# Kernel optimization log

Measured on AMD Instinct MI355X. Metric: run time of the kernel, lower is better.

Reference implementation:

```python
import jax, jax.numpy as jnp
import numpy as np

B, H, W = 16, 16, 16
L = 32          # in_capsules
O = 32          # out_capsules
P = 16          # p_size
PD = 4          # p_dim = sqrt(p_size)
ETA = 1.0


def setup_inputs() -> dict:
    key = jax.random.key(0)
    k1, k2, k3 = jax.random.split(key, 3)
    # [B, H, W, L*(P+1)]: first L*P channels are poses, last L are activations in [0,1]
    input_tensor = jax.random.uniform(k1, (B, H, W, L * (P + 1)), dtype=jnp.float32)
    # transform weights: [L, O, 4, 4] (kernel_size=1, shared over spatial positions)
    weights = jax.random.normal(k2, (L, O, PD, PD), dtype=jnp.float32) / np.sqrt(PD)
    activation_bias = jax.random.uniform(k3, (O,), dtype=jnp.float32)
    return {"input_tensor": input_tensor, "weights": weights,
            "activation_bias": activation_bias}


def reference(input_tensor, weights, activation_bias):
    Bs, Hh, Ww, _ = input_tensor.shape
    M = Hh * Ww
    # split poses / activations
    poses = input_tensor[..., : L * P].reshape(Bs, M, L, PD, PD)   # [B, M, L, 4, 4]
    acts = input_tensor[..., L * P:].reshape(Bs, M * L)            # [B, N]
    # votes[b, (m,l), o] = pose[b,m,l] @ W[l,o]  (shared transform, repeated over M)
    votes = jnp.einsum('bmlij,lojk->bmloik', poses, weights)
    votes = votes.reshape(Bs, M * L, O, P)                         # [B, N, O, 16]
    # weight votes by input activations and group per output capsule
    Y = (acts[:, :, None, None] * votes).transpose(0, 2, 1, 3)     # [B, O, N, 16]
    # top-1 right singular vector via gram matrix eigendecomposition (detached)
    gram = jnp.einsum('bonp,bonq->bopq', Y, Y)                     # [B, O, 16, 16]
    _, V = jnp.linalg.eigh(jax.lax.stop_gradient(gram))            # ascending eigvals
    pose_out = V[..., -1]                                          # [B, O, 16]
    # agreement: ||Y u||^2 / ||Y||_F^2
    yu = jnp.einsum('bonp,bop->bon', Y, pose_out)                  # [B, O, N]
    ratio = (yu ** 2).sum(-1) / (Y ** 2).sum((-1, -2))             # [B, O]
    act_out = jax.nn.sigmoid(ETA * (ratio - activation_bias))      # [B, O]
    return act_out, pose_out
```

## Files before the change

### kernel.cpp

```cpp
#include <hip/hip_runtime.h>

#define B_ 16
#define L_ 32
#define O_ 32
#define M_ 256
#define CH_ 544


__device__ __forceinline__ float rl(float v, int lane) {
  return __int_as_float(__builtin_amdgcn_readlane(__float_as_int(v), lane));
}

__device__ __forceinline__ float sum16_rl(float v) {
  float s = rl(v, 0);
#pragma unroll
  for (int j = 1; j < 16; j++) s += rl(v, j);
  return s;
}

__device__ __forceinline__ float frcp(float x) { return __builtin_amdgcn_rcpf(x); }
__device__ __forceinline__ float frsq(float x) { return __builtin_amdgcn_rsqf(x); }


__device__ __forceinline__ float slapy2f(float x, float y) {
  float xa = fabsf(x), ya = fabsf(y);
  float w = fmaxf(xa, ya), z = fminf(xa, ya);
  if (z == 0.f) return w;
  float q = z * frcp(w);
  return w * sqrtf(1.f + q * q);
}

__device__ __forceinline__ void slartgf(float f, float g, float* c, float* s, float* r) {
  if (g == 0.f) { *c = 1.f; *s = 0.f; *r = f; }
  else if (f == 0.f) { *c = 0.f; *s = copysignf(1.f, g); *r = fabsf(g); }
  else {
    float t = f * f + g * g;
    float inv = frsq(t);
    float d = t * inv;
    *c = fabsf(f) * inv;
    *r = copysignf(d, f);
    *s = g * copysignf(inv, f);
  }
}

__device__ __forceinline__ void slaev2f(float a, float b, float c,
                                        float* rt1, float* rt2, float* cs1, float* sn1) {
  float sm = a + c, df = a - c;
  float adf = fabsf(df);
  float tb = b + b;
  float ab = fabsf(tb);
  float acmx, acmn;
  if (fabsf(a) > fabsf(c)) { acmx = a; acmn = c; } else { acmx = c; acmn = a; }
  float rt;
  if (adf > ab) { float q = ab / adf; rt = adf * sqrtf(1.f + q * q); }
  else if (adf < ab) { float q = adf / ab; rt = ab * sqrtf(1.f + q * q); }
  else rt = ab * sqrtf(2.f);
  int sgn1;
  if (sm < 0.f) { *rt1 = 0.5f * (sm - rt); sgn1 = -1; *rt2 = (acmx / *rt1) * acmn - (b / *rt1) * b; }
  else if (sm > 0.f) { *rt1 = 0.5f * (sm + rt); sgn1 = 1; *rt2 = (acmx / *rt1) * acmn - (b / *rt1) * b; }
  else { *rt1 = 0.5f * rt; *rt2 = -0.5f * rt; sgn1 = 1; }
  float cs; int sgn2;
  if (df >= 0.f) { cs = df + rt; sgn2 = 1; } else { cs = df - rt; sgn2 = -1; }
  float acs = fabsf(cs), c1, s1;
  if (acs > ab) { float ct = -tb / cs; s1 = 1.f / sqrtf(1.f + ct * ct); c1 = ct * s1; }
  else if (ab == 0.f) { c1 = 1.f; s1 = 0.f; }
  else { float tn = -cs / tb; c1 = 1.f / sqrtf(1.f + tn * tn); s1 = tn * c1; }
  if (sgn1 == sgn2) { float tn = c1; c1 = -s1; s1 = tn; }
  *cs1 = c1; *sn1 = s1;
}

__global__ __launch_bounds__(256) void moments_kernel(const float* __restrict__ in,
                                                      float* __restrict__ Tmom) {
  int bl = blockIdx.x;
  int b = bl >> 5, l = bl & 31;
  int t = threadIdx.x;
  int w = t >> 6, lane = t & 63;
  __shared__ __align__(16) float ut[4][16][68];
  const float* base = in + (size_t)b * (M_ * CH_);
  const float* row = base + (size_t)(w * 64 + lane) * CH_ + l * 16;
  float4 p0 = *(const float4*)(row + 0);
  float4 p1 = *(const float4*)(row + 4);
  float4 p2 = *(const float4*)(row + 8);
  float4 p3 = *(const float4*)(row + 12);
  float a = row[512 - l * 16 + l];
  float (*u)[68] = ut[w];
  u[0][lane] = a * p0.x;  u[1][lane] = a * p0.y;  u[2][lane] = a * p0.z;  u[3][lane] = a * p0.w;
  u[4][lane] = a * p1.x;  u[5][lane] = a * p1.y;  u[6][lane] = a * p1.z;  u[7][lane] = a * p1.w;
  u[8][lane] = a * p2.x;  u[9][lane] = a * p2.y;  u[10][lane] = a * p2.z; u[11][lane] = a * p2.w;
  u[12][lane] = a * p3.x; u[13][lane] = a * p3.y; u[14][lane] = a * p3.z; u[15][lane] = a * p3.w;
  asm volatile("" ::: "memory");
  int c = lane & 15, r0 = lane >> 4;
  float acc0 = 0.f, acc1 = 0.f, acc2 = 0.f, acc3 = 0.f;
#pragma unroll
  for (int m4 = 0; m4 < 64; m4 += 4) {
    float4 cv = *(const float4*)&u[c][m4];
    float4 a0 = *(const float4*)&u[r0][m4];
    float4 a1 = *(const float4*)&u[r0 + 4][m4];
    float4 a2 = *(const float4*)&u[r0 + 8][m4];
    float4 a3 = *(const float4*)&u[r0 + 12][m4];
    acc0 += a0.x * cv.x + a0.y * cv.y + a0.z * cv.z + a0.w * cv.w;
    acc1 += a1.x * cv.x + a1.y * cv.y + a1.z * cv.z + a1.w * cv.w;
    acc2 += a2.x * cv.x + a2.y * cv.y + a2.z * cv.z + a2.w * cv.w;
    acc3 += a3.x * cv.x + a3.y * cv.y + a3.z * cv.z + a3.w * cv.w;
  }
  float* dst = Tmom + ((size_t)bl * 4 + w) * 256;
  dst[r0 * 16 + c] = acc0;
  dst[(r0 + 4) * 16 + c] = acc1;
  dst[(r0 + 8) * 16 + c] = acc2;
  dst[(r0 + 12) * 16 + c] = acc3;
}

__global__ __launch_bounds__(64) void gram_eig_kernel(const float* __restrict__ Tmom,
                                                      const float* __restrict__ Wt,
                                                      const float* __restrict__ bias,
                                                      float* __restrict__ out) {
  int bo = blockIdx.x;
  int b = bo >> 5, o = bo & 31;
  int lane = threadIdx.x;

  __shared__ __align__(16) float4 Wall4[128];
  __shared__ __align__(16) float4 Tsh4[4 * 18];
  __shared__ float A[16][17];
  __shared__ __align__(16) float Zt[16][16];

  const float4* Wt4 = (const float4*)Wt;
#pragma unroll
  for (int k = 0; k < 2; k++) {
    int idx = lane + 64 * k;
    int l = idx >> 2, part = idx & 3;
    Wall4[idx] = Wt4[(l * 32 + o) * 4 + part];
  }
  asm volatile("" ::: "memory");

  int p = lane >> 2;
  int i_ = p >> 2, k_ = p & 3;
  int i2 = lane & 3;
  float gx = 0.f, gy = 0.f, gz = 0.f, gw = 0.f;
  const float4* T4b = (const float4*)Tmom + (size_t)(b * 32) * 4 * 64;
  const float* WallF = (const float*)Wall4;
  float4 tc0 = T4b[0 * 64 + lane], tc1 = T4b[1 * 64 + lane];
  float4 tc2 = T4b[2 * 64 + lane], tc3 = T4b[3 * 64 + lane];
  float4 tn0 = T4b[4 * 64 + lane], tn1 = T4b[5 * 64 + lane];
  float4 tn2 = T4b[6 * 64 + lane], tn3 = T4b[7 * 64 + lane];
  for (int l = 0; l < 32; l++) {
    float4 tsum;
    tsum.x = (tc0.x + tc1.x) + (tc2.x + tc3.x);
    tsum.y = (tc0.y + tc1.y) + (tc2.y + tc3.y);
    tsum.z = (tc0.z + tc1.z) + (tc2.z + tc3.z);
    tsum.w = (tc0.w + tc1.w) + (tc2.w + tc3.w);
    Tsh4[(lane >> 4) * 18 + (lane & 15)] = tsum;
    asm volatile("" ::: "memory");
    tc0 = tn0; tc1 = tn1; tc2 = tn2; tc3 = tn3;
    if (l + 2 < 32) {
      const float4* nb = T4b + (size_t)(l + 2) * 4 * 64;
      tn0 = nb[0 * 64 + lane]; tn1 = nb[1 * 64 + lane];
      tn2 = nb[2 * 64 + lane]; tn3 = nb[3 * 64 + lane];
    }
    float4 wq0 = Wall4[l * 4 + 0], wq1 = Wall4[l * 4 + 1];
    float4 wq2 = Wall4[l * 4 + 2], wq3 = Wall4[l * 4 + 3];
#pragma unroll
    for (int jj = 0; jj < 4; jj++) {
      float4 trow = Tsh4[i_ * 18 + jj * 4 + i2];
      float ux = trow.x * wq0.x + trow.y * wq1.x + trow.z * wq2.x + trow.w * wq3.x;
      float uy = trow.x * wq0.y + trow.y * wq1.y + trow.z * wq2.y + trow.w * wq3.y;
      float uz = trow.x * wq0.z + trow.y * wq1.z + trow.z * wq2.z + trow.w * wq3.z;
      float uw = trow.x * wq0.w + trow.y * wq1.w + trow.z * wq2.w + trow.w * wq3.w;
      float wk = WallF[l * 16 + jj * 4 + k_];
      gx += wk * ux; gy += wk * uy; gz += wk * uz; gw += wk * uw;
    }
    asm volatile("" ::: "memory");
  }
  {
    int q0 = i2 * 4;
    A[p][q0 + 0] = gx; A[p][q0 + 1] = gy; A[p][q0 + 2] = gz; A[p][q0 + 3] = gw;
  }
  asm volatile("" ::: "memory");

  int c16 = lane & 15;
  float a[16];
#pragma unroll
  for (int r = 0; r < 16; r++) a[r] = A[r][c16];

  float trace;
  {
    float diag = 0.f;
#pragma unroll
    for (int r = 0; r < 16; r++) if (c16 == r) diag = a[r];
    trace = sum16_rl((lane < 16) ? diag : 0.f);
  }

  float dreg = 0.f, ereg = 0.f, taureg = 0.f;
  float hv[14];
#pragma unroll
  for (int i = 0; i < 15; i++) {
    float cn = 0.f;
#pragma unroll
    for (int r = i + 2; r < 16; r++) cn += a[r] * a[r];
    float xn2 = rl(cn, i);
    float alpha = rl(a[i + 1], i);
    float taui = 0.f;
    float vc = 0.f;
    if (xn2 == 0.f) {
      if (lane == i) ereg = alpha;
    } else {
      float xnorm = sqrtf(xn2);
      float beta = -copysignf(slapy2f(alpha, xnorm), alpha);
      taui = (beta - alpha) / beta;
      float rs = 1.f / (alpha - beta);
      if (lane == i) ereg = beta;
      vc = (lane == i + 1) ? 1.f : ((lane >= i + 2 && lane < 16) ? a[i] * rs : 0.f);
      float vb[16];
#pragma unroll
      for (int r = i + 1; r < 16; r++) vb[r] = rl(vc, r);
      float acc = 0.f;
#pragma unroll
      for (int r = i + 1; r < 16; r++) acc += a[r] * vb[r];
      float wc = (lane >= i + 1 && lane < 16) ? taui * acc : 0.f;
      float wb[16];
#pragma unroll
      for (int r = i + 1; r < 16; r++) wb[r] = rl(wc, r);
      float dot = 0.f;
#pragma unroll
      for (int r = i + 1; r < 16; r++) dot += vb[r] * wb[r];
      float alph2 = -0.5f * taui * dot;
      wc += alph2 * vc;
#pragma unroll
      for (int r = i + 1; r < 16; r++) wb[r] += alph2 * vb[r];
#pragma unroll
      for (int r = i + 1; r < 16; r++) a[r] -= vb[r] * wc + wb[r] * vc;
    }
    if (i < 14) hv[i] = vc;
    if (lane == i) taureg = taui;
  }
#pragma unroll
  for (int r = 0; r < 16; r++) if (c16 == r) dreg = a[r];
  if (lane >= 16) dreg = 0.f;

  float z[16];
#pragma unroll
  for (int r = 0; r < 16; r++) z[r] = (lane == r) ? 1.f : 0.f;
#pragma unroll
  for (int i = 13; i >= 0; i--) {
    float taui = rl(taureg, i);
    if (taui != 0.f) {
      float vbq[16];
      float s = 0.f;
#pragma unroll
      for (int r = i + 1; r < 16; r++) { vbq[r] = rl(hv[i], r); s += vbq[r] * z[r]; }
      s *= taui;
#pragma unroll
      for (int r = i + 1; r < 16; r++) z[r] -= vbq[r] * s;
    }
  }
  if (lane < 16) {
    float4* zt4 = (float4*)&Zt[lane][0];
    zt4[0] = make_float4(z[0], z[1], z[2], z[3]);
    zt4[1] = make_float4(z[4], z[5], z[6], z[7]);
    zt4[2] = make_float4(z[8], z[9], z[10], z[11]);
    zt4[3] = make_float4(z[12], z[13], z[14], z[15]);
  }
  asm volatile("" ::: "memory");

  const float eps = 5.9604645e-08f;
  const float eps2 = eps * eps;
  const float safmin = 1.17549435e-38f;
  int l1 = 0, jtot = 0;
  const int nmaxit = 480;
  float dsh = __shfl(dreg, (lane + 1) & 63, 64);

  while (l1 < 16) {
    if (l1 > 0) { if (lane == l1 - 1) ereg = 0.f; }
    bool co = (lane < 15) &&
              ((ereg == 0.f) ||
               (fabsf(ereg) <= __builtin_amdgcn_sqrtf(fabsf(dreg)) *
                                   __builtin_amdgcn_sqrtf(fabsf(dsh)) * eps));
    unsigned long long bm = __ballot(co) & ~((1ull << l1) - 1ull);
    int m = bm ? (__ffsll(bm) - 1) : 15;
    if (m < 15) { if (lane == m) ereg = 0.f; }
    int l = l1, lend = m;
    l1 = m + 1;
    if (lend == l) continue;
    {
      float dl = rl(dreg, l), dle = rl(dreg, lend);
      if (fabsf(dle) < fabsf(dl)) { int tq = l; l = lend; lend = tq; }
    }

    if (lend > l) {
      for (;;) {
        bool cj = (lane < 15) && ((ereg * ereg) <= eps2 * fabsf(dreg) * fabsf(dsh) + safmin);
        int mq;
        if (l != lend) {
          unsigned long long bb2 = __ballot(cj) & ((1ull << lend) - 1ull) & ~((1ull << l) - 1ull);
          mq = bb2 ? (__ffsll(bb2) - 1) : lend;
        } else mq = lend;
        if (mq < lend) { if (lane == mq) ereg = 0.f; }
        if (mq == l) { l++; if (l <= lend) continue; break; }
        if (mq == l + 1) {
          float d_l = rl(dreg, l), e_l = rl(ereg, l), d_l1 = rl(dreg, l + 1);
          float rt1, rt2, cc, ss;
          slaev2f(d_l, e_l, d_l1, &rt1, &rt2, &cc, &ss);
          if (lane < 16) {
            float z1 = Zt[l + 1][lane], z0 = Zt[l][lane];
            Zt[l + 1][lane] = cc * z1 - ss * z0;
            Zt[l][lane] = ss * z1 + cc * z0;
          }
          if (lane == l) { dreg = rt1; ereg = 0.f; dsh = rt2; }
          if (lane == l + 1) dreg = rt2;
          if (lane == l - 1) dsh = rt1;
          l += 2; if (l <= lend) continue; break;
        }
        if (jtot == nmaxit) break;
        jtot++;
        float d0 = dreg, e0 = ereg;
        float pp = rl(d0, l);
        float e_lv = rl(e0, l);
        float gg = (rl(d0, l + 1) - pp) * 0.5f * frcp(e_lv);
        float rr = slapy2f(gg, 1.f);
        gg = rl(d0, mq) - pp + e_lv * frcp(gg + copysignf(rr, gg));
        float ss_ = 1.f, cc_ = 1.f;
        pp = 0.f;
        float zc = (lane < 16) ? Zt[mq][lane] : 0.f;
        float znxt = (lane < 16) ? Zt[mq - 1][lane] : 0.f;
        for (int i = mq - 1; i >= l; i--) {
          float z0 = znxt;
          if (i > l) znxt = (lane < 16) ? Zt[i - 1][lane] : 0.f;
          float e_i = rl(e0, i), d_i = rl(d0, i), d_i1 = rl(d0, i + 1);
          float ff = ss_ * e_i, bb = cc_ * e_i;
          slartgf(gg, ff, &cc_, &ss_, &rr);
          if (i != mq - 1) { if (lane == i + 1) ereg = rr; }
          gg = d_i1 - pp;
          rr = (d_i - gg) * ss_ + 2.f * cc_ * bb;
          pp = ss_ * rr;
          float dnew = gg + pp;
          if (lane == i + 1) dreg = dnew;
          if (lane == i) dsh = dnew;
          gg = cc_ * rr - bb;
          if (lane < 16) Zt[i + 1][lane] = cc_ * zc + ss_ * z0;
          zc = -ss_ * zc + cc_ * z0;
        }
        if (lane < 16) Zt[l][lane] = zc;
        float dlv = rl(d0, l) - pp;
        if (lane == l) { dreg = dlv; ereg = gg; }
        if (lane == l - 1) dsh = dlv;
      }
    } else {
      for (;;) {
        bool cj = (lane < 15) && ((ereg * ereg) <= eps2 * fabsf(dreg) * fabsf(dsh) + safmin);
        int mq;
        if (l != lend) {
          unsigned long long bb2 = __ballot(cj) & ((1ull << l) - 1ull) & ~((1ull << lend) - 1ull);
          mq = bb2 ? (63 - __clzll(bb2) + 1) : lend;
        } else mq = lend;
        if (mq > lend) { if (lane == mq - 1) ereg = 0.f; }
        if (mq == l) { l--; if (l >= lend) continue; break; }
        if (mq == l - 1) {
          float d_lm1 = rl(dreg, l - 1), e_lm1 = rl(ereg, l - 1), d_l = rl(dreg, l);
          float rt1, rt2, cc, ss;
          slaev2f(d_lm1, e_lm1, d_l, &rt1, &rt2, &cc, &ss);
          if (lane < 16) {
            float z1 = Zt[l][lane], z0 = Zt[l - 1][lane];
            Zt[l][lane] = cc * z1 - ss * z0;
            Zt[l - 1][lane] = ss * z1 + cc * z0;
          }
          if (lane == l - 1) { dreg = rt1; ereg = 0.f; dsh = rt2; }
          if (lane == l) dreg = rt2;
          if (lane == l - 2) dsh = rt1;
          l -= 2; if (l >= lend) continue; break;
        }
        if (jtot == nmaxit) break;
        jtot++;
        float d0 = dreg, e0 = ereg;
        float pp = rl(d0, l);
        float e_lm1 = rl(e0, l - 1);
        float gg = (rl(d0, l - 1) - pp) * 0.5f * frcp(e_lm1);
        float rr = slapy2f(gg, 1.f);
        gg = rl(d0, mq) - pp + e_lm1 * frcp(gg + copysignf(rr, gg));
        float ss_ = 1.f, cc_ = 1.f;
        pp = 0.f;
        float zc = (lane < 16) ? Zt[mq][lane] : 0.f;
        float znxt = (lane < 16) ? Zt[mq + 1][lane] : 0.f;
        for (int i = mq; i <= l - 1; i++) {
          float z1 = znxt;
          if (i < l - 1) znxt = (lane < 16) ? Zt[i + 2][lane] : 0.f;
          float e_i = rl(e0, i), d_i = rl(d0, i), d_i1 = rl(d0, i + 1);
          float ff = ss_ * e_i, bb = cc_ * e_i;
          slartgf(gg, ff, &cc_, &ss_, &rr);
          if (i != mq) { if (lane == i - 1) ereg = rr; }
          gg = d_i - pp;
          rr = (d_i1 - gg) * ss_ + 2.f * cc_ * bb;
          pp = ss_ * rr;
          float dnew = gg + pp;
          if (lane == i) dreg = dnew;
          if (lane == i - 1) dsh = dnew;
          gg = cc_ * rr - bb;
          if (lane < 16) Zt[i][lane] = ss_ * z1 + cc_ * zc;
          zc = cc_ * z1 - ss_ * zc;
        }
        if (lane < 16) Zt[l][lane] = zc;
        float dlv = rl(d0, l) - pp;
        if (lane == l) dreg = dlv;
        if (lane == l - 1) { ereg = gg; dsh = dlv; }
      }
    }
  }
  asm volatile("" ::: "memory");

  float mx = rl(dreg, 0);
  int k = 0;
#pragma unroll
  for (int j = 1; j < 16; j++) {
    float dj = rl(dreg, j);
    if (dj > mx) { mx = dj; k = j; }
  }
  float ratio = mx / trace;
  float act = 1.f / (1.f + expf(-(ratio - bias[o])));
  if (lane < 16) out[512 + bo * 16 + lane] = Zt[k][lane];
  if (lane == 0) out[bo] = act;
}

extern "C" void kernel_launch(void* const* d_in, const int* in_sizes, int n_in,
                              void* d_out, int out_size, void* d_ws, size_t ws_size,
                              hipStream_t stream) {
  const float* in = (const float*)d_in[0];
  const float* w = (const float*)d_in[1];
  const float* bias = (const float*)d_in[2];
  float* out = (float*)d_out;
  float* Tmom = (float*)d_ws;

  moments_kernel<<<B_ * L_, 256, 0, stream>>>(in, Tmom);
  gram_eig_kernel<<<B_ * O_, 64, 0, stream>>>(Tmom, w, bias, out);
}
```

Baseline: 132.6 us.

## Keep eigenvector matrix in registers, reduce moment partials in-block, branchless Givens

```diff
diff --git a/kernel.cpp b/kernel.cpp
--- a/kernel.cpp
+++ b/kernel.cpp
@@ -25,22 +25,22 @@
 __device__ __forceinline__ float slapy2f(float x, float y) {
   float xa = fabsf(x), ya = fabsf(y);
   float w = fmaxf(xa, ya), z = fminf(xa, ya);
-  if (z == 0.f) return w;
   float q = z * frcp(w);
-  return w * sqrtf(1.f + q * q);
+  float res = w * sqrtf(1.f + q * q);
+  return (z == 0.f) ? w : res;
 }
 
 __device__ __forceinline__ void slartgf(float f, float g, float* c, float* s, float* r) {
-  if (g == 0.f) { *c = 1.f; *s = 0.f; *r = f; }
-  else if (f == 0.f) { *c = 0.f; *s = copysignf(1.f, g); *r = fabsf(g); }
-  else {
-    float t = f * f + g * g;
-    float inv = frsq(t);
-    float d = t * inv;
-    *c = fabsf(f) * inv;
-    *r = copysignf(d, f);
-    *s = g * copysignf(inv, f);
-  }
+  float t = f * f + g * g;
+  float inv = frsq(t);
+  float d = t * inv;
+  float cg = fabsf(f) * inv;
+  float rg = copysignf(d, f);
+  float sg = g * copysignf(inv, f);
+  bool g0 = (g == 0.f), f0 = (f == 0.f);
+  *c = g0 ? 1.f : (f0 ? 0.f : cg);
+  *s = g0 ? 0.f : (f0 ? copysignf(1.f, g) : sg);
+  *r = g0 ? f : (f0 ? fabsf(g) : rg);
 }
 
 __device__ __forceinline__ void slaev2f(float a, float b, float c,
@@ -76,6 +76,7 @@
   int t = threadIdx.x;
   int w = t >> 6, lane = t & 63;
   __shared__ __align__(16) float ut[4][16][68];
+  __shared__ float red[4][16][16];
   const float* base = in + (size_t)b * (M_ * CH_);
   const float* row = base + (size_t)(w * 64 + lane) * CH_ + l * 16;
   float4 p0 = *(const float4*)(row + 0);
@@ -103,11 +104,14 @@
     acc2 += a2.x * cv.x + a2.y * cv.y + a2.z * cv.z + a2.w * cv.w;
     acc3 += a3.x * cv.x + a3.y * cv.y + a3.z * cv.z + a3.w * cv.w;
   }
-  float* dst = Tmom + ((size_t)bl * 4 + w) * 256;
-  dst[r0 * 16 + c] = acc0;
-  dst[(r0 + 4) * 16 + c] = acc1;
-  dst[(r0 + 8) * 16 + c] = acc2;
-  dst[(r0 + 12) * 16 + c] = acc3;
+  red[w][r0][c] = acc0;
+  red[w][r0 + 4][c] = acc1;
+  red[w][r0 + 8][c] = acc2;
+  red[w][r0 + 12][c] = acc3;
+  __syncthreads();
+  int rr_ = t >> 4, cc_ = t & 15;
+  float s = (red[0][rr_][cc_] + red[1][rr_][cc_]) + (red[2][rr_][cc_] + red[3][rr_][cc_]);
+  Tmom[bl * 256 + t] = s;
 }
 
 __global__ __launch_bounds__(64) void gram_eig_kernel(const float* __restrict__ Tmom,
@@ -123,6 +127,8 @@
   __shared__ float A[16][17];
   __shared__ __align__(16) float Zt[16][16];
 
+  float biasv = bias[o];
+
   const float4* Wt4 = (const float4*)Wt;
 #pragma unroll
   for (int k = 0; k < 2; k++) {
@@ -136,26 +142,15 @@
   int i_ = p >> 2, k_ = p & 3;
   int i2 = lane & 3;
   float gx = 0.f, gy = 0.f, gz = 0.f, gw = 0.f;
-  const float4* T4b = (const float4*)Tmom + (size_t)(b * 32) * 4 * 64;
+  const float4* T4 = (const float4*)(Tmom + (size_t)(b * 32) * 256);
   const float* WallF = (const float*)Wall4;
-  float4 tc0 = T4b[0 * 64 + lane], tc1 = T4b[1 * 64 + lane];
-  float4 tc2 = T4b[2 * 64 + lane], tc3 = T4b[3 * 64 + lane];
-  float4 tn0 = T4b[4 * 64 + lane], tn1 = T4b[5 * 64 + lane];
-  float4 tn2 = T4b[6 * 64 + lane], tn3 = T4b[7 * 64 + lane];
+  float4 t0 = T4[0 * 64 + lane], t1 = T4[1 * 64 + lane];
+  float4 t2 = T4[2 * 64 + lane], t3 = T4[3 * 64 + lane];
   for (int l = 0; l < 32; l++) {
-    float4 tsum;
-    tsum.x = (tc0.x + tc1.x) + (tc2.x + tc3.x);
-    tsum.y = (tc0.y + tc1.y) + (tc2.y + tc3.y);
-    tsum.z = (tc0.z + tc1.z) + (tc2.z + tc3.z);
-    tsum.w = (tc0.w + tc1.w) + (tc2.w + tc3.w);
-    Tsh4[(lane >> 4) * 18 + (lane & 15)] = tsum;
+    Tsh4[(lane >> 4) * 18 + (lane & 15)] = t0;
     asm volatile("" ::: "memory");
-    tc0 = tn0; tc1 = tn1; tc2 = tn2; tc3 = tn3;
-    if (l + 2 < 32) {
-      const float4* nb = T4b + (size_t)(l + 2) * 4 * 64;
-      tn0 = nb[0 * 64 + lane]; tn1 = nb[1 * 64 + lane];
-      tn2 = nb[2 * 64 + lane]; tn3 = nb[3 * 64 + lane];
-    }
+    t0 = t1; t1 = t2; t2 = t3;
+    if (l + 4 < 32) t3 = T4[(l + 4) * 64 + lane];
     float4 wq0 = Wall4[l * 4 + 0], wq1 = Wall4[l * 4 + 1];
     float4 wq2 = Wall4[l * 4 + 2], wq3 = Wall4[l * 4 + 3];
 #pragma unroll
@@ -260,6 +255,10 @@
     zt4[3] = make_float4(z[12], z[13], z[14], z[15]);
   }
   asm volatile("" ::: "memory");
+
+  float zz[16];
+#pragma unroll
+  for (int k2 = 0; k2 < 16; k2++) zz[k2] = Zt[k2][c16];
 
   const float eps = 5.9604645e-08f;
   const float eps2 = eps * eps;
@@ -299,10 +298,11 @@
           float d_l = rl(dreg, l), e_l = rl(ereg, l), d_l1 = rl(dreg, l + 1);
           float rt1, rt2, cc, ss;
           slaev2f(d_l, e_l, d_l1, &rt1, &rt2, &cc, &ss);
-          if (lane < 16) {
-            float z1 = Zt[l + 1][lane], z0 = Zt[l][lane];
-            Zt[l + 1][lane] = cc * z1 - ss * z0;
-            Zt[l][lane] = ss * z1 + cc * z0;
+#pragma unroll
+          for (int k = 0; k < 15; k++) if (k == l) {
+            float z1 = zz[k + 1], z0v = zz[k];
+            zz[k + 1] = cc * z1 - ss * z0v;
+            zz[k] = ss * z1 + cc * z0v;
           }
           if (lane == l) { dreg = rt1; ereg = 0.f; dsh = rt2; }
           if (lane == l + 1) dreg = rt2;
@@ -319,26 +319,25 @@
         gg = rl(d0, mq) - pp + e_lv * frcp(gg + copysignf(rr, gg));
         float ss_ = 1.f, cc_ = 1.f;
         pp = 0.f;
-        float zc = (lane < 16) ? Zt[mq][lane] : 0.f;
-        float znxt = (lane < 16) ? Zt[mq - 1][lane] : 0.f;
-        for (int i = mq - 1; i >= l; i--) {
-          float z0 = znxt;
-          if (i > l) znxt = (lane < 16) ? Zt[i - 1][lane] : 0.f;
-          float e_i = rl(e0, i), d_i = rl(d0, i), d_i1 = rl(d0, i + 1);
-          float ff = ss_ * e_i, bb = cc_ * e_i;
-          slartgf(gg, ff, &cc_, &ss_, &rr);
-          if (i != mq - 1) { if (lane == i + 1) ereg = rr; }
-          gg = d_i1 - pp;
-          rr = (d_i - gg) * ss_ + 2.f * cc_ * bb;
-          pp = ss_ * rr;
-          float dnew = gg + pp;
-          if (lane == i + 1) dreg = dnew;
-          if (lane == i) dsh = dnew;
-          gg = cc_ * rr - bb;
-          if (lane < 16) Zt[i + 1][lane] = cc_ * zc + ss_ * z0;
-          zc = -ss_ * zc + cc_ * z0;
+#pragma unroll
+        for (int i = 14; i >= 0; i--) {
+          if (i <= mq - 1 && i >= l) {
+            float e_i = rl(e0, i), d_i = rl(d0, i), d_i1 = rl(d0, i + 1);
+            float ff = ss_ * e_i, bb = cc_ * e_i;
+            slartgf(gg, ff, &cc_, &ss_, &rr);
+            if (i != mq - 1) { if (lane == i + 1) ereg = rr; }
+            gg = d_i1 - pp;
+            rr = (d_i - gg) * ss_ + 2.f * cc_ * bb;
+            pp = ss_ * rr;
+            float dnew = gg + pp;
+            if (lane == i + 1) dreg = dnew;
+            if (lane == i) dsh = dnew;
+            gg = cc_ * rr - bb;
+            float z1 = zz[i + 1], z0v = zz[i];
+            zz[i + 1] = cc_ * z1 + ss_ * z0v;
+            zz[i] = -ss_ * z1 + cc_ * z0v;
+          }
         }
-        if (lane < 16) Zt[l][lane] = zc;
         float dlv = rl(d0, l) - pp;
         if (lane == l) { dreg = dlv; ereg = gg; }
         if (lane == l - 1) dsh = dlv;
@@ -357,10 +356,11 @@
           float d_lm1 = rl(dreg, l - 1), e_lm1 = rl(ereg, l - 1), d_l = rl(dreg, l);
           float rt1, rt2, cc, ss;
           slaev2f(d_lm1, e_lm1, d_l, &rt1, &rt2, &cc, &ss);
-          if (lane < 16) {
-            float z1 = Zt[l][lane], z0 = Zt[l - 1][lane];
-            Zt[l][lane] = cc * z1 - ss * z0;
-            Zt[l - 1][lane] = ss * z1 + cc * z0;
+#pragma unroll
+          for (int k = 0; k < 15; k++) if (k == l - 1) {
+            float z1 = zz[k + 1], z0v = zz[k];
+            zz[k + 1] = cc * z1 - ss * z0v;
+            zz[k] = ss * z1 + cc * z0v;
           }
           if (lane == l - 1) { dreg = rt1; ereg = 0.f; dsh = rt2; }
           if (lane == l) dreg = rt2;
@@ -377,33 +377,31 @@
         gg = rl(d0, mq) - pp + e_lm1 * frcp(gg + copysignf(rr, gg));
         float ss_ = 1.f, cc_ = 1.f;
         pp = 0.f;
-        float zc = (lane < 16) ? Zt[mq][lane] : 0.f;
-        float znxt = (lane < 16) ? Zt[mq + 1][lane] : 0.f;
-        for (int i = mq; i <= l - 1; i++) {
-          float z1 = znxt;
-          if (i < l - 1) znxt = (lane < 16) ? Zt[i + 2][lane] : 0.f;
-          float e_i = rl(e0, i), d_i = rl(d0, i), d_i1 = rl(d0, i + 1);
-          float ff = ss_ * e_i, bb = cc_ * e_i;
-          slartgf(gg, ff, &cc_, &ss_, &rr);
-          if (i != mq) { if (lane == i - 1) ereg = rr; }
-          gg = d_i - pp;
-          rr = (d_i1 - gg) * ss_ + 2.f * cc_ * bb;
-          pp = ss_ * rr;
-          float dnew = gg + pp;
-          if (lane == i) dreg = dnew;
-          if (lane == i - 1) dsh = dnew;
-          gg = cc_ * rr - bb;
-          if (lane < 16) Zt[i][lane] = ss_ * z1 + cc_ * zc;
-          zc = cc_ * z1 - ss_ * zc;
+#pragma unroll
+        for (int i = 0; i <= 14; i++) {
+          if (i >= mq && i <= l - 1) {
+            float e_i = rl(e0, i), d_i = rl(d0, i), d_i1 = rl(d0, i + 1);
+            float ff = ss_ * e_i, bb = cc_ * e_i;
+            slartgf(gg, ff, &cc_, &ss_, &rr);
+            if (i != mq) { if (lane == i - 1) ereg = rr; }
+            gg = d_i - pp;
+            rr = (d_i1 - gg) * ss_ + 2.f * cc_ * bb;
+            pp = ss_ * rr;
+            float dnew = gg + pp;
+            if (lane == i) dreg = dnew;
+            if (lane == i - 1) dsh = dnew;
+            gg = cc_ * rr - bb;
+            float z1 = zz[i + 1], z0v = zz[i];
+            zz[i + 1] = cc_ * z1 - ss_ * z0v;
+            zz[i] = ss_ * z1 + cc_ * z0v;
+          }
         }
-        if (lane < 16) Zt[l][lane] = zc;
         float dlv = rl(d0, l) - pp;
         if (lane == l) dreg = dlv;
         if (lane == l - 1) { ereg = gg; dsh = dlv; }
       }
     }
   }
-  asm volatile("" ::: "memory");
 
   float mx = rl(dreg, 0);
   int k = 0;
@@ -413,8 +411,11 @@
     if (dj > mx) { mx = dj; k = j; }
   }
   float ratio = mx / trace;
-  float act = 1.f / (1.f + expf(-(ratio - bias[o])));
-  if (lane < 16) out[512 + bo * 16 + lane] = Zt[k][lane];
+  float act = 1.f / (1.f + expf(-(ratio - biasv)));
+  float zk = zz[0];
+#pragma unroll
+  for (int j = 1; j < 16; j++) zk = (k == j) ? zz[j] : zk;
+  if (lane < 16) out[512 + bo * 16 + lane] = zk;
   if (lane == 0) out[bo] = act;
 }
 
```

Result: no change. 131.1 us (-1.1%).
